# Kernel optimization log

Hardware: AMD Instinct MI355X
Metric: run time of the kernel (lower is better)

Reference implementation:

```python
import jax, jax.numpy as jnp
import numpy as np

_K_MASK = float(jnp.finfo(jnp.float32).min)
EPS = 1e-6
B, T, D = 2, 2048, 2048
NH, NKV, HD = 16, 4, 128


def _rope_tables(key):
    # Standard RoPE tables: (B, T, HD) with [freqs, freqs] layout (rotate_half convention)
    inv_freq = 1.0 / (10000.0 ** (np.arange(0, HD, 2, dtype=np.float32) / HD))  # (HD/2,)
    pos = np.arange(T, dtype=np.float32)
    freqs = np.einsum('t,f->tf', pos, inv_freq)              # (T, HD/2)
    emb = np.concatenate([freqs, freqs], axis=-1)            # (T, HD)
    cos = jnp.broadcast_to(jnp.cos(emb)[None], (B, T, HD))
    sin = jnp.broadcast_to(jnp.sin(emb)[None], (B, T, HD))
    return cos, sin


def setup_inputs() -> dict:
    key = jax.random.key(0)
    ks = jax.random.split(key, 6)
    s = 0.02
    cos, sin = _rope_tables(key)
    return {
        'x': jax.random.normal(ks[0], (B, T, D), jnp.float32),
        'cos': cos,
        'sin': sin,
        'wq': jax.random.normal(ks[1], (D, NH * HD * 2), jnp.float32) * s,
        'wk': jax.random.normal(ks[2], (D, NKV * HD), jnp.float32) * s,
        'wv': jax.random.normal(ks[3], (D, NKV * HD), jnp.float32) * s,
        'wo': jax.random.normal(ks[4], (NH * HD, D), jnp.float32) * s,
        'q_norm_w': jnp.ones((HD,), jnp.float32),
        'k_norm_w': jnp.ones((HD,), jnp.float32),
        'segment_ids': jnp.ones((B, T), jnp.int32),
        'position_ids': jnp.broadcast_to(jnp.arange(T, dtype=jnp.int32)[None], (B, T)),
    }


def _rmsnorm(x, w):
    var = jnp.mean(jnp.square(x.astype(jnp.float32)), axis=-1, keepdims=True)
    return (x.astype(jnp.float32) * jax.lax.rsqrt(var + EPS)).astype(x.dtype) * w


def _rotate_half(x):
    x1, x2 = jnp.split(x, 2, axis=-1)
    return jnp.concatenate([-x2, x1], axis=-1)


def _apply_rope(q, k, cos, sin):
    # q: (B, NH, T, HD), k: (B, NKV, T, HD), cos/sin: (B, T, HD)
    c = cos[:, None, :, :]
    s = sin[:, None, :, :]
    q = q * c + _rotate_half(q) * s
    k = k * c + _rotate_half(k) * s
    return q, k


def reference(x, cos, sin, wq, wk, wv, wo, q_norm_w, k_norm_w, segment_ids, position_ids):
    Bx, Tx, _ = x.shape
    n_rep = NH // NKV
    scale = HD ** -0.5

    q_out = (x @ wq).reshape(Bx, Tx, NH, HD * 2)
    query, gate = jnp.split(q_out, 2, axis=-1)         # each (B, T, NH, HD)
    gate = gate.reshape(Bx, Tx, -1)                    # (B, T, NH*HD)
    query = _rmsnorm(query, q_norm_w).transpose(0, 2, 1, 3)   # (B, NH, T, HD)
    key = _rmsnorm((x @ wk).reshape(Bx, Tx, NKV, HD), k_norm_w).transpose(0, 2, 1, 3)
    value = (x @ wv).reshape(Bx, Tx, NKV, HD).transpose(0, 2, 1, 3)

    query, key = _apply_rope(query, key, cos, sin)
    if n_rep > 1:
        key = jnp.repeat(key, n_rep, axis=1)
        value = jnp.repeat(value, n_rep, axis=1)

    attn_logits = jnp.einsum('bhqd,bhkd->bhqk', query, key) * scale
    causal = position_ids[:, :, None] >= position_ids[:, None, :]
    seg = segment_ids[:, :, None] == segment_ids[:, None, :]
    mask = (causal & seg)[:, None, :, :]
    attn_logits = jnp.where(mask, attn_logits, _K_MASK)
    attn_weights = jax.nn.softmax(attn_logits.astype(jnp.float32), axis=-1).astype(attn_logits.dtype)
    attn_out = jnp.einsum('bhqk,bhkd->bhqd', attn_weights, value)
    attn_out = attn_out.transpose(0, 2, 1, 3).reshape(Bx, Tx, -1)  # (B, T, NH*HD)
    attn_out = attn_out * jax.nn.sigmoid(gate)
    return attn_out @ wo
```

## Files before the change

### kernel.cpp

```cpp
#include <hip/hip_runtime.h>

#define AS1 __attribute__((address_space(1)))
#define AS3 __attribute__((address_space(3)))

typedef __bf16 bf16x8 __attribute__((ext_vector_type(8)));
typedef float f32x4 __attribute__((ext_vector_type(4)));
typedef float f32x16 __attribute__((ext_vector_type(16)));
typedef unsigned short us8 __attribute__((ext_vector_type(8)));
typedef unsigned int u32x4 __attribute__((ext_vector_type(4)));

static constexpr int T_ = 2048;
static constexpr int NH_ = 16;
static constexpr int NKV_ = 4;
static constexpr int HD_ = 128;
static constexpr int NQKV_ = 5120;
static constexpr float SL2E_ = 0.12751744f;

static __device__ __forceinline__ unsigned short f2b(float f) {
  unsigned u = __builtin_bit_cast(unsigned, f);
  u += 0x7fffu + ((u >> 16) & 1u);
  return (unsigned short)(u >> 16);
}
static __device__ __forceinline__ float b2f(unsigned short h) {
  unsigned u = ((unsigned)h) << 16;
  return __builtin_bit_cast(float, u);
}
static __device__ __forceinline__ void load_lds16(const void* g, void* l) {
  __builtin_amdgcn_global_load_lds((const AS1 unsigned int*)g, (AS3 unsigned int*)l, 16, 0, 0);
}
static __device__ __forceinline__ f32x4 mfma16(bf16x8 a, bf16x8 b, f32x4 c) {
  return __builtin_amdgcn_mfma_f32_16x16x32_bf16(a, b, c, 0, 0, 0);
}
static __device__ __forceinline__ f32x16 mfma32(bf16x8 a, bf16x8 b, f32x16 c) {
  return __builtin_amdgcn_mfma_f32_32x32x16_bf16(a, b, c, 0, 0, 0);
}
static __device__ __forceinline__ unsigned cvtpk(float lo, float hi) {
  unsigned r;
  asm("v_cvt_pk_bf16_f32 %0, %1, %2" : "=v"(r) : "v"(lo), "v"(hi));
  return r;
}
static __device__ __forceinline__ void pl32swap(unsigned& a, unsigned& b) {
  asm("v_permlane32_swap_b32 %0, %1" : "+v"(a), "+v"(b));
}
#define S_BARRIER() asm volatile("s_barrier" ::: "memory")
#define VMCNT(n) asm volatile("s_waitcnt vmcnt(" #n ")" ::: "memory")

__global__ __launch_bounds__(256) void conv_bf16_kernel(
    const float* __restrict__ src, unsigned short* __restrict__ dst, int n) {
  int i = (blockIdx.x * 256 + threadIdx.x) * 4;
  if (i >= n) return;
  float4 v = *(const float4*)(src + i);
  ushort4 o;
  o.x = f2b(v.x); o.y = f2b(v.y); o.z = f2b(v.z); o.w = f2b(v.w);
  *(ushort4*)(dst + i) = o;
}

__global__ void tconv_kernel(const float* __restrict__ src, unsigned short* __restrict__ dst,
                             int R, int C, int roff) {
  __shared__ float tile[32][33];
  const int c0 = blockIdx.x * 32, r0 = blockIdx.y * 32;
#pragma unroll
  for (int j = 0; j < 32; j += 8)
    tile[threadIdx.y + j][threadIdx.x] =
        src[(size_t)(r0 + threadIdx.y + j) * C + c0 + threadIdx.x];
  __syncthreads();
#pragma unroll
  for (int j = 0; j < 32; j += 8)
    dst[(size_t)(roff + c0 + threadIdx.y + j) * R + r0 + threadIdx.x] =
        f2b(tile[threadIdx.x][threadIdx.y + j]);
}

__global__ void vtrans_kernel(const unsigned short* __restrict__ qkv,
                              unsigned short* __restrict__ Vt) {
  __shared__ unsigned short tile[32][33];
  const int bh = blockIdx.z;
  const int b = bh >> 2, vh = bh & 3;
  const int d0 = blockIdx.x * 32, t0 = blockIdx.y * 32;
#pragma unroll
  for (int j = 0; j < 32; j += 8) {
    const int t = t0 + threadIdx.y + j;
    tile[threadIdx.y + j][threadIdx.x] =
        qkv[(size_t)(b * T_ + t) * NQKV_ + 4608 + vh * 128 + d0 + threadIdx.x];
  }
  __syncthreads();
  unsigned short* dst = Vt + (size_t)bh * HD_ * T_;
#pragma unroll
  for (int j = 0; j < 32; j += 8)
    dst[(size_t)(d0 + threadIdx.y + j) * T_ + t0 + threadIdx.x] =
        tile[threadIdx.x][threadIdx.y + j];
}

template <int BF16OUT>
__global__ __launch_bounds__(512, 2) void gemm_bt8_kernel(
    const unsigned short* __restrict__ A, const unsigned short* __restrict__ Bt,
    void* __restrict__ Cv, int K, int N) {
  __shared__ __align__(16) unsigned short As[3][128 * 64];
  __shared__ __align__(16) unsigned short Bs[3][256 * 64];
  const int tid = threadIdx.x;
  const int wid = tid >> 6, lane = tid & 63;
  const int lq = lane & 15, lg = lane >> 4;
  const int l8 = lane >> 3, s8 = lane & 7;
  const int wr = wid >> 2, wc = wid & 3;
  const int brow = blockIdx.y * 128, bcol = blockIdx.x * 256;

  f32x4 acc[4][4];
#pragma unroll
  for (int m = 0; m < 4; ++m)
#pragma unroll
    for (int n = 0; n < 4; ++n) acc[m][n] = (f32x4){0.f, 0.f, 0.f, 0.f};

  auto STAGE_HALF = [&](int t, int b3t, int half) {
    const int k0 = t * 64;
    {
      const int ca = wid + half * 8;
      const int row = ca * 8 + l8;
      load_lds16(A + (size_t)(brow + row) * K + k0 + ((s8 ^ (row & 7)) << 3),
                 &As[b3t][ca << 9]);
    }
#pragma unroll
    for (int j = 0; j < 2; ++j) {
      const int cb = wid + half * 16 + (j << 3);
      const int row = cb * 8 + l8;
      load_lds16(Bt + (size_t)(bcol + row) * K + k0 + ((s8 ^ (row & 7)) << 3),
                 &Bs[b3t][cb << 9]);
    }
  };
  auto PHASE_READS = [&](int b3, int ks, bf16x8* a, bf16x8* bb) {
#pragma unroll
    for (int m = 0; m < 4; ++m) {
      const int r = wr * 64 + m * 16 + lq;
      a[m] = *(const bf16x8*)&As[b3][r * 64 + (((ks * 4 + lg) ^ (r & 7)) << 3)];
    }
#pragma unroll
    for (int n = 0; n < 4; ++n) {
      const int r = wc * 64 + n * 16 + lq;
      bb[n] = *(const bf16x8*)&Bs[b3][r * 64 + (((ks * 4 + lg) ^ (r & 7)) << 3)];
    }
  };
  auto DO_MFMA = [&](bf16x8* a, bf16x8* bb) {
    __builtin_amdgcn_s_setprio(1);
#pragma unroll
    for (int m = 0; m < 4; ++m)
#pragma unroll
      for (int n = 0; n < 4; ++n) acc[m][n] = mfma16(a[m], bb[n], acc[m][n]);
    __builtin_amdgcn_s_setprio(0);
  };

  STAGE_HALF(0, 0, 0); STAGE_HALF(0, 0, 1);
  STAGE_HALF(1, 1, 0); STAGE_HALF(1, 1, 1);
  VMCNT(6);
  S_BARRIER();

  int b3 = 0;
  for (int t = 0; t < 32; ++t) {
    const int b3p2 = b3 < 1 ? b3 + 2 : b3 - 1;
    bf16x8 a[4], bb[4];
    PHASE_READS(b3, 0, a, bb);
    if (t < 30) STAGE_HALF(t + 2, b3p2, 0);
    S_BARRIER();
    __builtin_amdgcn_sched_barrier(0);
    DO_MFMA(a, bb);
    S_BARRIER();
    PHASE_READS(b3, 1, a, bb);
    if (t < 30) STAGE_HALF(t + 2, b3p2, 1);
    if (t < 30) {
      VMCNT(6);
    } else if (t == 30) {
      VMCNT(0);
    }
    S_BARRIER();
    __builtin_amdgcn_sched_barrier(0);
    DO_MFMA(a, bb);
    if (t < 31) S_BARRIER();
    b3 = b3 < 2 ? b3 + 1 : 0;
  }
#pragma unroll
  for (int m = 0; m < 4; ++m)
#pragma unroll
    for (int n = 0; n < 4; ++n)
#pragma unroll
      for (int r = 0; r < 4; ++r) {
        const size_t idx =
            (size_t)(brow + wr * 64 + m * 16 + lg * 4 + r) * N + bcol + wc * 64 + n * 16 + lq;
        if constexpr (BF16OUT) {
          ((unsigned short*)Cv)[idx] = f2b(acc[m][n][r]);
        } else {
          ((float*)Cv)[idx] = acc[m][n][r];
        }
      }
}

__global__ __launch_bounds__(256) void postproc_kernel(
    const unsigned short* __restrict__ qkv, const float* __restrict__ cosT,
    const float* __restrict__ sinT, const float* __restrict__ qnw,
    const float* __restrict__ knw, unsigned short* __restrict__ Qg,
    unsigned short* __restrict__ Kg) {
  const int row = blockIdx.x;
  const int b = row >> 11, t = row & 2047;
  const unsigned short* src = qkv + (size_t)row * NQKV_;
  const int tid = threadIdx.x;
  const int sub = tid & 15;
  const int i0 = sub * 8;
  const bool lo = sub < 8;

  float cs[8], sn[8];
#pragma unroll
  for (int j = 0; j < 8; ++j) {
    cs[j] = cosT[(size_t)row * HD_ + i0 + j];
    sn[j] = sinT[(size_t)row * HD_ + i0 + j];
  }
  {
    const int h = tid >> 4;
    us8 qv = *(const us8*)(src + h * 256 + i0);
    float q[8], ss = 0.f;
#pragma unroll
    for (int j = 0; j < 8; ++j) { q[j] = b2f(qv[j]); ss += q[j] * q[j]; }
    ss += __shfl_xor(ss, 1); ss += __shfl_xor(ss, 2);
    ss += __shfl_xor(ss, 4); ss += __shfl_xor(ss, 8);
    const float rms = rsqrtf(ss * (1.f / 128.f) + 1e-6f);
    float qn[8];
#pragma unroll
    for (int j = 0; j < 8; ++j) qn[j] = q[j] * rms * qnw[i0 + j];
    float pr[8];
#pragma unroll
    for (int j = 0; j < 8; ++j) pr[j] = __shfl_xor(qn[j], 8);
    us8 ov;
#pragma unroll
    for (int j = 0; j < 8; ++j) ov[j] = f2b(qn[j] * cs[j] + (lo ? -pr[j] : pr[j]) * sn[j]);
    *(us8*)(Qg + ((size_t)(b * NH_ + h) * T_ + t) * HD_ + i0) = ov;
  }
  if (tid < 64) {
    const int kh = tid >> 4;
    us8 kv8 = *(const us8*)(src + 4096 + kh * 128 + i0);
    float k[8], ss = 0.f;
#pragma unroll
    for (int j = 0; j < 8; ++j) { k[j] = b2f(kv8[j]); ss += k[j] * k[j]; }
    ss += __shfl_xor(ss, 1); ss += __shfl_xor(ss, 2);
    ss += __shfl_xor(ss, 4); ss += __shfl_xor(ss, 8);
    const float rms = rsqrtf(ss * (1.f / 128.f) + 1e-6f);
    float kn[8];
#pragma unroll
    for (int j = 0; j < 8; ++j) kn[j] = k[j] * rms * knw[i0 + j];
    float pr[8];
#pragma unroll
    for (int j = 0; j < 8; ++j) pr[j] = __shfl_xor(kn[j], 8);
    us8 ov;
#pragma unroll
    for (int j = 0; j < 8; ++j) ov[j] = f2b(kn[j] * cs[j] + (lo ? -pr[j] : pr[j]) * sn[j]);
    *(us8*)(Kg + ((size_t)(b * NKV_ + kh) * T_ + t) * HD_ + i0) = ov;
  }
}

__global__ __launch_bounds__(256, 2) void attn_kernel(
    const unsigned short* __restrict__ Qg, const unsigned short* __restrict__ Kg,
    const unsigned short* __restrict__ Vt, const unsigned short* __restrict__ qkv,
    unsigned short* __restrict__ attnb) {
  __shared__ __align__(16) char smem[65536];
  const int i = blockIdx.x;
  const int xi = (i >> 3) & 15;
  const int grp = (i & 7) + ((i >> 7) << 3);
  const int h = grp & 15, b = grp >> 4;
  const int qt = b ? (15 - xi) : xi;
  const int kh = h >> 2;
  const int tid = threadIdx.x, wid = tid >> 6, lane = tid & 63;
  const int lq = lane & 31, hi = lane >> 5;
  const int q0 = qt * 128;
  const int qbase = q0 + wid * 32;
  const int qrow = qbase + lq;

  bf16x8 qf[8];
  const unsigned short* qptr = Qg + ((size_t)(b * NH_ + h) * T_ + qrow) * HD_;
#pragma unroll
  for (int t = 0; t < 8; ++t) qf[t] = *(const bf16x8*)(qptr + t * 16 + hi * 8);

  const char* Kbase = (const char*)(Kg + (size_t)(b * NKV_ + kh) * T_ * HD_);
  const char* Vbase = (const char*)(Vt + (size_t)(b * NKV_ + kh) * HD_ * T_);

  f32x16 o[4];
#pragma unroll
  for (int d = 0; d < 4; ++d)
#pragma unroll
    for (int r = 0; r < 16; ++r) o[d][r] = 0.f;
  float m_r = -1e30f, l_r = 0.f;
  const int nt = 2 * qt + 2;

  auto STAGE = [&](int tt, int c) {
    const int t0 = tt * 64;
    char* kd = smem + c * 32768;
    char* vd = kd + 16384;
#pragma unroll
    for (int j = 0; j < 4; ++j) {
      const int ch = j * 4 + wid;
      const int kv = ch * 4 + (lane >> 4);
      load_lds16(Kbase + (size_t)(t0 + kv) * 256 + (((lane & 15) ^ (kv & 7)) << 4),
                 kd + ch * 1024);
      const int dv = ch * 8 + (lane >> 3);
      load_lds16(Vbase + (size_t)dv * (T_ * 2) + (size_t)t0 * 2 +
                     (((lane & 7) ^ (dv & 7)) << 4),
                 vd + ch * 1024);
    }
  };

  STAGE(0, 0);
  __syncthreads();
  int cur = 0;
  for (int tt = 0; tt < nt; ++tt) {
    const int t0 = tt * 64;
    if (tt + 1 < nt) STAGE(tt + 1, cur ^ 1);
    if (t0 <= qbase + 31) {
      const char* kd = smem + cur * 32768;
      const char* vd = kd + 16384;
      f32x16 sA, sB;
#pragma unroll
      for (int r = 0; r < 16; ++r) { sA[r] = 0.f; sB[r] = 0.f; }
      __builtin_amdgcn_s_setprio(1);
#pragma unroll
      for (int t = 0; t < 8; ++t) {
        const int sw = t * 2 + hi;
        bf16x8 ka = *(const bf16x8*)(kd + lq * 256 + ((sw ^ (lq & 7)) << 4));
        bf16x8 kb = *(const bf16x8*)(kd + (lq + 32) * 256 + ((sw ^ (lq & 7)) << 4));
        sA = mfma32(ka, qf[t], sA);
        sB = mfma32(kb, qf[t], sB);
      }
      __builtin_amdgcn_s_setprio(0);
      float p[32];
      float mx = -1e30f;
      const bool anymask = (t0 + 63 > qbase);
#pragma unroll
      for (int r = 0; r < 16; ++r) {
        const int kv = (r & 3) + ((r >> 2) << 3) + hi * 4;
        float vA = sA[r] * SL2E_;
        float vB = sB[r] * SL2E_;
        if (anymask) {
          if (t0 + kv > qrow) vA = -1e30f;
          if (t0 + kv + 32 > qrow) vB = -1e30f;
        }
        p[r] = vA; p[16 + r] = vB;
        mx = fmaxf(mx, fmaxf(vA, vB));
      }
      mx = fmaxf(mx, __shfl_xor(mx, 32));
      const float mn = fmaxf(m_r, mx);
      const float al = exp2f(m_r - mn);
      float sum = 0.f;
#pragma unroll
      for (int j = 0; j < 32; ++j) { p[j] = exp2f(p[j] - mn); sum += p[j]; }
      sum += __shfl_xor(sum, 32);
      l_r = l_r * al + sum;
      m_r = mn;
#pragma unroll
      for (int d = 0; d < 4; ++d)
#pragma unroll
        for (int r = 0; r < 16; ++r) o[d][r] *= al;
      bf16x8 pf[4];
#pragma unroll
      for (int kt = 0; kt < 4; ++kt) {
        const float* pp = p + kt * 8;
        unsigned a0 = cvtpk(pp[0], pp[1]);
        unsigned a1 = cvtpk(pp[2], pp[3]);
        unsigned b0 = cvtpk(pp[4], pp[5]);
        unsigned b1 = cvtpk(pp[6], pp[7]);
        pl32swap(a0, b0);
        pl32swap(a1, b1);
        u32x4 w = {a0, a1, b0, b1};
        pf[kt] = __builtin_bit_cast(bf16x8, w);
      }
      __builtin_amdgcn_s_setprio(1);
#pragma unroll
      for (int dt = 0; dt < 4; ++dt) {
        const int d = dt * 32 + lq;
#pragma unroll
        for (int kt = 0; kt < 4; ++kt) {
          bf16x8 vf = *(const bf16x8*)(vd + d * 128 + (((kt * 2 + hi) ^ (d & 7)) << 4));
          o[dt] = mfma32(vf, pf[kt], o[dt]);
        }
      }
      __builtin_amdgcn_s_setprio(0);
    }
    __syncthreads();
    cur ^= 1;
  }
  const float inv = 1.f / l_r;
  const unsigned short* grow = qkv + (size_t)(b * T_ + qrow) * NQKV_ + h * 256 + 128;
  unsigned short* orow = attnb + (size_t)(b * T_ + qrow) * (NH_ * HD_) + h * HD_;
#pragma unroll
  for (int dt = 0; dt < 4; ++dt)
#pragma unroll
    for (int g = 0; g < 4; ++g) {
      const int d0 = dt * 32 + g * 8 + hi * 4;
      ushort4 gv = *(const ushort4*)(grow + d0);
      ushort4 ov;
      ov.x = f2b(o[dt][g * 4 + 0] * inv / (1.f + __expf(-b2f(gv.x))));
      ov.y = f2b(o[dt][g * 4 + 1] * inv / (1.f + __expf(-b2f(gv.y))));
      ov.z = f2b(o[dt][g * 4 + 2] * inv / (1.f + __expf(-b2f(gv.z))));
      ov.w = f2b(o[dt][g * 4 + 3] * inv / (1.f + __expf(-b2f(gv.w))));
      *(ushort4*)(orow + d0) = ov;
    }
}

extern "C" void kernel_launch(void* const* d_in, const int* in_sizes, int n_in,
                              void* d_out, int out_size, void* d_ws, size_t ws_size,
                              hipStream_t stream) {
  (void)in_sizes; (void)n_in; (void)out_size; (void)ws_size;
  const float* x    = (const float*)d_in[0];
  const float* cosT = (const float*)d_in[1];
  const float* sinT = (const float*)d_in[2];
  const float* wq   = (const float*)d_in[3];
  const float* wk   = (const float*)d_in[4];
  const float* wv   = (const float*)d_in[5];
  const float* wo   = (const float*)d_in[6];
  const float* qnw  = (const float*)d_in[7];
  const float* knw  = (const float*)d_in[8];
  float* out = (float*)d_out;
  char* ws = (char*)d_ws;

  constexpr size_t OFF_XB    = 0;
  constexpr size_t OFF_WQKVT = OFF_XB    + (size_t)4096 * 2048 * 2;
  constexpr size_t OFF_WOT   = OFF_WQKVT + (size_t)5120 * 2048 * 2;
  constexpr size_t OFF_QKV   = OFF_WOT   + (size_t)2048 * 2048 * 2;
  constexpr size_t OFF_QG    = OFF_QKV   + (size_t)4096 * 5120 * 2;
  constexpr size_t OFF_KG    = OFF_QG    + (size_t)2 * 16 * 2048 * 128 * 2;
  constexpr size_t OFF_VT    = OFF_KG    + (size_t)2 * 4 * 2048 * 128 * 2;
  constexpr size_t OFF_ATTNB = OFF_VT    + (size_t)2 * 4 * 128 * 2048 * 2;

  unsigned short* xb    = (unsigned short*)(ws + OFF_XB);
  unsigned short* wqkvT = (unsigned short*)(ws + OFF_WQKVT);
  unsigned short* woT   = (unsigned short*)(ws + OFF_WOT);
  unsigned short* qkv   = (unsigned short*)(ws + OFF_QKV);
  unsigned short* Qg    = (unsigned short*)(ws + OFF_QG);
  unsigned short* Kg    = (unsigned short*)(ws + OFF_KG);
  unsigned short* Vt    = (unsigned short*)(ws + OFF_VT);
  unsigned short* attnb = (unsigned short*)(ws + OFF_ATTNB);

  const int nX = 4096 * 2048;
  conv_bf16_kernel<<<nX / 4 / 256, 256, 0, stream>>>(x, xb, nX);
  tconv_kernel<<<dim3(4096 / 32, 2048 / 32), dim3(32, 8), 0, stream>>>(wq, wqkvT, 2048, 4096, 0);
  tconv_kernel<<<dim3(512 / 32, 2048 / 32), dim3(32, 8), 0, stream>>>(wk, wqkvT, 2048, 512, 4096);
  tconv_kernel<<<dim3(512 / 32, 2048 / 32), dim3(32, 8), 0, stream>>>(wv, wqkvT, 2048, 512, 4608);
  tconv_kernel<<<dim3(2048 / 32, 2048 / 32), dim3(32, 8), 0, stream>>>(wo, woT, 2048, 2048, 0);

  gemm_bt8_kernel<1><<<dim3(5120 / 256, 4096 / 128), 512, 0, stream>>>(
      xb, wqkvT, (void*)qkv, 2048, 5120);

  postproc_kernel<<<4096, 256, 0, stream>>>(qkv, cosT, sinT, qnw, knw, Qg, Kg);
  vtrans_kernel<<<dim3(128 / 32, 2048 / 32, 8), dim3(32, 8), 0, stream>>>(qkv, Vt);

  attn_kernel<<<512, 256, 0, stream>>>(Qg, Kg, Vt, qkv, attnb);

  gemm_bt8_kernel<0><<<dim3(2048 / 256, 4096 / 128), 512, 0, stream>>>(
      attnb, woT, (void*)out, 2048, 2048);
}
```

Baseline: 264.3 us.

## Add dedicated 256x320-tile QKV GEMM with XCD-aware block mapping and interleaved pipeline

```diff
diff --git a/kernel.cpp b/kernel.cpp
--- a/kernel.cpp
+++ b/kernel.cpp
@@ -88,6 +88,135 @@
   for (int j = 0; j < 32; j += 8)
     dst[(size_t)(d0 + threadIdx.y + j) * T_ + t0 + threadIdx.x] =
         tile[threadIdx.x][threadIdx.y + j];
+}
+
+__global__ __launch_bounds__(512, 2) void gemm1_kernel(
+    const unsigned short* __restrict__ A, const unsigned short* __restrict__ Bt,
+    unsigned short* __restrict__ C, int K, int N) {
+  __shared__ __align__(16) unsigned short As[2][256 * 64];
+  __shared__ __align__(16) unsigned short Bs[2][320 * 64];
+  const int bid = blockIdx.x;
+  const int xcd = bid & 7, c = bid >> 3;
+  const int brow = (((xcd & 1) << 3) | (c & 7)) * 256;
+  const int bcol = (((xcd >> 1) << 2) | (c >> 3)) * 320;
+  const int tid = threadIdx.x, wid = tid >> 6, lane = tid & 63;
+  const int lq = lane & 15, lg = lane >> 4;
+  const int wr = wid >> 2, wc = wid & 3;
+  const int srow = lane >> 3, spc = lane & 7;
+  const int ssw = (spc ^ srow) << 3;
+  const int sw0 = (lg ^ (lq & 7)) << 3;
+  const int sw1 = ((4 + lg) ^ (lq & 7)) << 3;
+
+  f32x4 acc[8][5];
+#pragma unroll
+  for (int m = 0; m < 8; ++m)
+#pragma unroll
+    for (int n = 0; n < 5; ++n) acc[m][n] = (f32x4){0.f, 0.f, 0.f, 0.f};
+
+  auto STAGE_A = [&](int t) {
+    const int k0 = t << 6, p = t & 1;
+#pragma unroll
+    for (int j = 0; j < 4; ++j) {
+      const int ch = wid * 4 + j;
+      load_lds16(A + (size_t)(brow + ch * 8 + srow) * K + k0 + ssw, &As[p][ch << 9]);
+    }
+  };
+  auto STAGE_B = [&](int t, int j0, int j1) {
+    const int k0 = t << 6, p = t & 1;
+    for (int j = j0; j < j1; ++j) {
+      const int ch = wid * 5 + j;
+      load_lds16(Bt + (size_t)(bcol + ch * 8 + srow) * K + k0 + ssw, &Bs[p][ch << 9]);
+    }
+  };
+  auto RD_A = [&](int p, int m, int ks) -> bf16x8 {
+    return *(const bf16x8*)&As[p][(wr * 128 + m * 16 + lq) * 64 + (ks ? sw1 : sw0)];
+  };
+  auto RD_B = [&](int p, int n, int ks) -> bf16x8 {
+    return *(const bf16x8*)&Bs[p][(wc * 80 + n * 16 + lq) * 64 + (ks ? sw1 : sw0)];
+  };
+
+  STAGE_A(0); STAGE_B(0, 0, 5);
+  STAGE_A(1); STAGE_B(1, 0, 5);
+  VMCNT(9);
+  S_BARRIER();
+
+  const int NT = K >> 6;
+  for (int t = 0; t < NT; ++t) {
+    const int p = t & 1;
+    bf16x8 aL[4][2], aH[4][2], bL[2][2], bH[3][2];
+#pragma unroll
+    for (int m = 0; m < 4; ++m) { aL[m][0] = RD_A(p, m, 0); aL[m][1] = RD_A(p, m, 1); }
+#pragma unroll
+    for (int n = 0; n < 2; ++n) { bL[n][0] = RD_B(p, n, 0); bL[n][1] = RD_B(p, n, 1); }
+    S_BARRIER();
+    __builtin_amdgcn_sched_barrier(0);
+    __builtin_amdgcn_s_setprio(1);
+#pragma unroll
+    for (int m = 0; m < 4; ++m)
+#pragma unroll
+      for (int n = 0; n < 2; ++n) {
+        acc[m][n] = mfma16(aL[m][0], bL[n][0], acc[m][n]);
+        acc[m][n] = mfma16(aL[m][1], bL[n][1], acc[m][n]);
+      }
+    __builtin_amdgcn_s_setprio(0);
+    S_BARRIER();
+#pragma unroll
+    for (int n = 0; n < 3; ++n) { bH[n][0] = RD_B(p, n + 2, 0); bH[n][1] = RD_B(p, n + 2, 1); }
+    S_BARRIER();
+    __builtin_amdgcn_sched_barrier(0);
+    __builtin_amdgcn_s_setprio(1);
+#pragma unroll
+    for (int m = 0; m < 4; ++m)
+#pragma unroll
+      for (int n = 0; n < 3; ++n) {
+        acc[m][n + 2] = mfma16(aL[m][0], bH[n][0], acc[m][n + 2]);
+        acc[m][n + 2] = mfma16(aL[m][1], bH[n][1], acc[m][n + 2]);
+      }
+    __builtin_amdgcn_s_setprio(0);
+    S_BARRIER();
+#pragma unroll
+    for (int m = 0; m < 4; ++m) { aH[m][0] = RD_A(p, m + 4, 0); aH[m][1] = RD_A(p, m + 4, 1); }
+    if (t < NT - 2) STAGE_B(t + 2, 0, 3);
+    S_BARRIER();
+    __builtin_amdgcn_sched_barrier(0);
+    __builtin_amdgcn_s_setprio(1);
+#pragma unroll
+    for (int m = 0; m < 4; ++m)
+#pragma unroll
+      for (int n = 0; n < 3; ++n) {
+        acc[m + 4][n + 2] = mfma16(aH[m][0], bH[n][0], acc[m + 4][n + 2]);
+        acc[m + 4][n + 2] = mfma16(aH[m][1], bH[n][1], acc[m + 4][n + 2]);
+      }
+    __builtin_amdgcn_s_setprio(0);
+    S_BARRIER();
+    if (t < NT - 2) {
+      STAGE_B(t + 2, 3, 5);
+      STAGE_A(t + 2);
+      VMCNT(9);
+    } else if (t == NT - 2) {
+      VMCNT(0);
+    }
+    S_BARRIER();
+    __builtin_amdgcn_sched_barrier(0);
+    __builtin_amdgcn_s_setprio(1);
+#pragma unroll
+    for (int m = 0; m < 4; ++m)
+#pragma unroll
+      for (int n = 0; n < 2; ++n) {
+        acc[m + 4][n] = mfma16(aH[m][0], bL[n][0], acc[m + 4][n]);
+        acc[m + 4][n] = mfma16(aH[m][1], bL[n][1], acc[m + 4][n]);
+      }
+    __builtin_amdgcn_s_setprio(0);
+    S_BARRIER();
+  }
+#pragma unroll
+  for (int m = 0; m < 8; ++m)
+#pragma unroll
+    for (int n = 0; n < 5; ++n)
+#pragma unroll
+      for (int r = 0; r < 4; ++r)
+        C[(size_t)(brow + wr * 128 + m * 16 + lg * 4 + r) * N + bcol + wc * 80 + n * 16 + lq] =
+            f2b(acc[m][n][r]);
 }
 
 template <int BF16OUT>
@@ -438,8 +567,7 @@
   tconv_kernel<<<dim3(512 / 32, 2048 / 32), dim3(32, 8), 0, stream>>>(wv, wqkvT, 2048, 512, 4608);
   tconv_kernel<<<dim3(2048 / 32, 2048 / 32), dim3(32, 8), 0, stream>>>(wo, woT, 2048, 2048, 0);
 
-  gemm_bt8_kernel<1><<<dim3(5120 / 256, 4096 / 128), 512, 0, stream>>>(
-      xb, wqkvT, (void*)qkv, 2048, 5120);
+  gemm1_kernel<<<256, 512, 0, stream>>>(xb, wqkvT, qkv, 2048, 5120);
 
   postproc_kernel<<<4096, 256, 0, stream>>>(qkv, cosT, sinT, qnw, knw, Qg, Kg);
   vtrans_kernel<<<dim3(128 / 32, 2048 / 32, 8), dim3(32, 8), 0, stream>>>(qkv, Vt);
```

Result: slower. 308.6 us (+16.8%).

## Fuse V transpose into QKV GEMM epilogue and skip redundant softmax rescales

Applied to the files above, without the earlier changes.

```diff
diff --git a/kernel.cpp b/kernel.cpp
--- a/kernel.cpp
+++ b/kernel.cpp
@@ -70,30 +70,10 @@
         f2b(tile[threadIdx.x][threadIdx.y + j]);
 }
 
-__global__ void vtrans_kernel(const unsigned short* __restrict__ qkv,
-                              unsigned short* __restrict__ Vt) {
-  __shared__ unsigned short tile[32][33];
-  const int bh = blockIdx.z;
-  const int b = bh >> 2, vh = bh & 3;
-  const int d0 = blockIdx.x * 32, t0 = blockIdx.y * 32;
-#pragma unroll
-  for (int j = 0; j < 32; j += 8) {
-    const int t = t0 + threadIdx.y + j;
-    tile[threadIdx.y + j][threadIdx.x] =
-        qkv[(size_t)(b * T_ + t) * NQKV_ + 4608 + vh * 128 + d0 + threadIdx.x];
-  }
-  __syncthreads();
-  unsigned short* dst = Vt + (size_t)bh * HD_ * T_;
-#pragma unroll
-  for (int j = 0; j < 32; j += 8)
-    dst[(size_t)(d0 + threadIdx.y + j) * T_ + t0 + threadIdx.x] =
-        tile[threadIdx.x][threadIdx.y + j];
-}
-
 template <int BF16OUT>
 __global__ __launch_bounds__(512, 2) void gemm_bt8_kernel(
     const unsigned short* __restrict__ A, const unsigned short* __restrict__ Bt,
-    void* __restrict__ Cv, int K, int N) {
+    void* __restrict__ Cv, unsigned short* __restrict__ Vt, int K, int N) {
   __shared__ __align__(16) unsigned short As[3][128 * 64];
   __shared__ __align__(16) unsigned short Bs[3][256 * 64];
   const int tid = threadIdx.x;
@@ -174,6 +154,25 @@
     if (t < 31) S_BARRIER();
     b3 = b3 < 2 ? b3 + 1 : 0;
   }
+  if constexpr (BF16OUT) {
+    if (bcol >= 4608) {
+#pragma unroll
+      for (int m = 0; m < 4; ++m) {
+        const int R0 = brow + wr * 64 + m * 16 + lg * 4;
+        const int bb2 = R0 >> 11, tt0 = R0 & 2047;
+#pragma unroll
+        for (int n = 0; n < 4; ++n) {
+          const int vcol = bcol + wc * 64 + n * 16 + lq - 4608;
+          const int vh = vcol >> 7, d = vcol & 127;
+          ushort4 v4;
+          v4.x = f2b(acc[m][n][0]); v4.y = f2b(acc[m][n][1]);
+          v4.z = f2b(acc[m][n][2]); v4.w = f2b(acc[m][n][3]);
+          *(ushort4*)&Vt[(size_t)((bb2 * 4 + vh) * 128 + d) * 2048 + tt0] = v4;
+        }
+      }
+      return;
+    }
+  }
 #pragma unroll
   for (int m = 0; m < 4; ++m)
 #pragma unroll
@@ -339,18 +338,21 @@
         mx = fmaxf(mx, fmaxf(vA, vB));
       }
       mx = fmaxf(mx, __shfl_xor(mx, 32));
-      const float mn = fmaxf(m_r, mx);
-      const float al = exp2f(m_r - mn);
+      if (!__all(mx <= m_r + 8.f)) {
+        const float mn = fmaxf(m_r, mx);
+        const float al = exp2f(m_r - mn);
+        l_r *= al;
+#pragma unroll
+        for (int d = 0; d < 4; ++d)
+#pragma unroll
+          for (int r = 0; r < 16; ++r) o[d][r] *= al;
+        m_r = mn;
+      }
       float sum = 0.f;
 #pragma unroll
-      for (int j = 0; j < 32; ++j) { p[j] = exp2f(p[j] - mn); sum += p[j]; }
+      for (int j = 0; j < 32; ++j) { p[j] = exp2f(p[j] - m_r); sum += p[j]; }
       sum += __shfl_xor(sum, 32);
-      l_r = l_r * al + sum;
-      m_r = mn;
-#pragma unroll
-      for (int d = 0; d < 4; ++d)
-#pragma unroll
-        for (int r = 0; r < 16; ++r) o[d][r] *= al;
+      l_r += sum;
       bf16x8 pf[4];
 #pragma unroll
       for (int kt = 0; kt < 4; ++kt) {
@@ -439,13 +441,12 @@
   tconv_kernel<<<dim3(2048 / 32, 2048 / 32), dim3(32, 8), 0, stream>>>(wo, woT, 2048, 2048, 0);
 
   gemm_bt8_kernel<1><<<dim3(5120 / 256, 4096 / 128), 512, 0, stream>>>(
-      xb, wqkvT, (void*)qkv, 2048, 5120);
+      xb, wqkvT, (void*)qkv, Vt, 2048, 5120);
 
   postproc_kernel<<<4096, 256, 0, stream>>>(qkv, cosT, sinT, qnw, knw, Qg, Kg);
-  vtrans_kernel<<<dim3(128 / 32, 2048 / 32, 8), dim3(32, 8), 0, stream>>>(qkv, Vt);
 
   attn_kernel<<<512, 256, 0, stream>>>(Qg, Kg, Vt, qkv, attnb);
 
   gemm_bt8_kernel<0><<<dim3(2048 / 256, 4096 / 128), 512, 0, stream>>>(
-      attnb, woT, (void*)out, 2048, 2048);
-}
+      attnb, woT, (void*)out, nullptr, 2048, 2048);
+}
```

Measured after the change: 264.3 us, median of 2. Within noise of the previous version (+0.0%).
